# Kernel optimization log

Hardware: AMD Instinct MI355X
Metric: run time of the kernel (lower is better)

Reference implementation:

```python
import jax, jax.numpy as jnp
import numpy as np

WS = 8          # window size
DIM = 512       # channels
NH = 16         # heads
HD = DIM // NH  # head dim = 32
N = WS * WS     # tokens per window = 64
NW = 64         # windows per image
B = 16          # images
BW = B * NW     # total windows = 1024
SCALE = HD ** -0.5


def _relative_position_index():
    # Swin relative position index, shape (N, N), values in [0, (2*WS-1)^2)
    coords = np.stack(np.meshgrid(np.arange(WS), np.arange(WS), indexing='ij'))  # (2, WS, WS)
    coords_flat = coords.reshape(2, -1)                                           # (2, N)
    rel = coords_flat[:, :, None] - coords_flat[:, None, :]                       # (2, N, N)
    rel = rel.transpose(1, 2, 0).astype(np.int32)                                 # (N, N, 2)
    rel[:, :, 0] += WS - 1
    rel[:, :, 1] += WS - 1
    rel[:, :, 0] *= 2 * WS - 1
    return jnp.asarray(rel.sum(-1))                                               # (N, N)


def setup_inputs() -> dict:
    key = jax.random.key(0)
    ks = jax.random.split(key, 7)
    x = jax.random.normal(ks[0], (BW, N, DIM), dtype=jnp.float32)
    mask = jax.random.normal(ks[1], (NW, N, N), dtype=jnp.float32)  # shift mask (additive)
    qkv_w = jax.random.normal(ks[2], (3 * DIM, DIM), dtype=jnp.float32) * 0.02
    qkv_b = jax.random.normal(ks[3], (3 * DIM,), dtype=jnp.float32) * 0.02
    rel_bias_table = jax.random.normal(ks[4], ((2 * WS - 1) ** 2, NH), dtype=jnp.float32) * 0.02
    proj_w = jax.random.normal(ks[5], (DIM, DIM), dtype=jnp.float32) * 0.02
    proj_b = jax.random.normal(ks[6], (DIM,), dtype=jnp.float32) * 0.02
    rel_index = _relative_position_index()
    return {"x": x, "mask": mask, "qkv_w": qkv_w, "qkv_b": qkv_b,
            "rel_bias_table": rel_bias_table, "proj_w": proj_w, "proj_b": proj_b,
            "rel_index": rel_index}


def reference(x, mask, qkv_w, qkv_b, rel_bias_table, proj_w, proj_b, rel_index):
    # qkv projection: (BW, N, 3*DIM) -> (3, BW, NH, N, HD)
    qkv = (x @ qkv_w.T + qkv_b).reshape(BW, N, 3, NH, HD).transpose(2, 0, 3, 1, 4)
    q, k, v = qkv[0], qkv[1], qkv[2]
    # scaled dot-product scores: (BW, NH, N, N)
    attn = jnp.einsum('bhnd,bhmd->bhnm', q * SCALE, k)
    # relative position bias: gather (N*N,) -> (N, N, NH) -> (NH, N, N)
    bias = rel_bias_table[rel_index.reshape(-1)].reshape(N, N, NH).transpose(2, 0, 1)
    attn = attn + bias[None]
    # shift mask: broadcast over images and heads
    attn = attn.reshape(B, NW, NH, N, N) + mask[None, :, None]
    attn = jax.nn.softmax(attn.reshape(BW, NH, N, N), axis=-1)
    # weighted values: (BW, NH, N, HD) -> (BW, N, DIM)
    out = jnp.einsum('bhnm,bhmd->bhnd', attn, v).transpose(0, 2, 1, 3).reshape(BW, N, DIM)
    return out @ proj_w.T + proj_b
```

## Files before the change

kernel.cpp:

```cpp
#include <hip/hip_runtime.h>
#include <hip/hip_bf16.h>

typedef __bf16 bf16;
typedef __bf16 bf16x4 __attribute__((ext_vector_type(4)));
typedef __bf16 bf16x8 __attribute__((ext_vector_type(8)));
typedef float  f32x4  __attribute__((ext_vector_type(4)));

#define AS1 __attribute__((address_space(1)))
#define AS3 __attribute__((address_space(3)))

__device__ __forceinline__ void gld_lds16(const void* g, void* l) {
    __builtin_amdgcn_global_load_lds((AS1 void*)g, (AS3 void*)l, 16, 0, 0);
}

__global__ void cvt_kernel(const float* __restrict__ in, bf16* __restrict__ out,
                           int n4) {
    for (long i = (long)blockIdx.x * blockDim.x + threadIdx.x; i < n4;
         i += (long)gridDim.x * blockDim.x) {
        f32x4 v = ((const f32x4*)in)[i];
        bf16x4 h;
#pragma unroll
        for (int e = 0; e < 4; ++e) h[e] = (bf16)v[e];
        ((bf16x4*)out)[i] = h;
    }
}

__global__ void bias_kernel(const int* __restrict__ rel_index,
                            const float* __restrict__ table,
                            float* __restrict__ bias) {
    int idx = blockIdx.x * 256 + threadIdx.x;
    int rc = idx & 4095;
    int h  = idx >> 12;
    bias[idx] = table[rel_index[rc] * 16 + h];
}

__global__ __launch_bounds__(256) void gemm1_qkv(
    const bf16* __restrict__ A, const bf16* __restrict__ B,
    const float* __restrict__ bias, bf16* __restrict__ Cq,
    bf16* __restrict__ Ckv)
{
    __shared__ __attribute__((aligned(16))) bf16 As[128 * 64];
    __shared__ __attribute__((aligned(16))) bf16 Bs[128 * 64];

    const int t    = threadIdx.x;
    const int w    = t >> 6;
    const int lane = t & 63;
    const int q    = lane >> 4;
    const int r16  = lane & 15;
    const int wm   = (w & 1) * 64;
    const int wn   = (w >> 1) * 64;
    const long bM  = (long)blockIdx.x * 128;
    const long bN  = (long)blockIdx.y * 128;

    const int sRow = lane >> 3;
    const int sCol = (lane & 7) * 8;

    f32x4 acc[4][4];
#pragma unroll
    for (int i = 0; i < 4; ++i)
#pragma unroll
        for (int j = 0; j < 4; ++j)
            acc[i][j] = f32x4{0.f, 0.f, 0.f, 0.f};

    for (int k0 = 0; k0 < 512; k0 += 64) {
#pragma unroll
        for (int it = 0; it < 4; ++it) {
            const int chunk = w * 4 + it;
            const int row   = chunk * 8 + sRow;
            gld_lds16(A + (bM + row) * 512L + k0 + sCol, As + chunk * 512);
            gld_lds16(B + (bN + row) * 512L + k0 + sCol, Bs + chunk * 512);
        }
        asm volatile("s_waitcnt vmcnt(0)" ::: "memory");
        __syncthreads();

#pragma unroll
        for (int ks = 0; ks < 2; ++ks) {
            bf16x8 av[4], bv[4];
#pragma unroll
            for (int i = 0; i < 4; ++i)
                av[i] = *(const bf16x8*)&As[(wm + i * 16 + r16) * 64 + ks * 32 + q * 8];
#pragma unroll
            for (int j = 0; j < 4; ++j)
                bv[j] = *(const bf16x8*)&Bs[(wn + j * 16 + r16) * 64 + ks * 32 + q * 8];
#pragma unroll
            for (int i = 0; i < 4; ++i)
#pragma unroll
                for (int j = 0; j < 4; ++j)
                    acc[i][j] = __builtin_amdgcn_mfma_f32_16x16x32_bf16(
                        av[i], bv[j], acc[i][j], 0, 0, 0);
        }
        __syncthreads();
    }

    const bool isQ = (bN < 512);
#pragma unroll
    for (int j = 0; j < 4; ++j) {
        const long colg = bN + wn + j * 16 + r16;
        const float bvv = bias[colg];
#pragma unroll
        for (int i = 0; i < 4; ++i) {
            const long row = bM + wm + i * 16 + q * 4;
#pragma unroll
            for (int r = 0; r < 4; ++r) {
                const float v = acc[i][j][r] + bvv;
                if (isQ) Cq [(row + r) * 512  + colg]         = (bf16)v;
                else     Ckv[(row + r) * 1024 + (colg - 512)] = (bf16)v;
            }
        }
    }
}

__global__ __launch_bounds__(256) void gemm2_proj(
    const bf16* __restrict__ A, const bf16* __restrict__ B,
    const float* __restrict__ bias, float* __restrict__ C)
{
    __shared__ __attribute__((aligned(16))) bf16 As[128 * 64];
    __shared__ __attribute__((aligned(16))) bf16 Bs[128 * 64];

    const int t    = threadIdx.x;
    const int w    = t >> 6;
    const int lane = t & 63;
    const int q    = lane >> 4;
    const int r16  = lane & 15;
    const int wm   = (w & 1) * 64;
    const int wn   = (w >> 1) * 64;
    const long bM  = (long)blockIdx.x * 128;
    const long bN  = (long)blockIdx.y * 128;

    const int sRow = lane >> 3;
    const int sCol = (lane & 7) * 8;

    f32x4 acc[4][4];
#pragma unroll
    for (int i = 0; i < 4; ++i)
#pragma unroll
        for (int j = 0; j < 4; ++j)
            acc[i][j] = f32x4{0.f, 0.f, 0.f, 0.f};

    for (int k0 = 0; k0 < 512; k0 += 64) {
#pragma unroll
        for (int it = 0; it < 4; ++it) {
            const int chunk = w * 4 + it;
            const int row   = chunk * 8 + sRow;
            gld_lds16(A + (bM + row) * 512L + k0 + sCol, As + chunk * 512);
            gld_lds16(B + (bN + row) * 512L + k0 + sCol, Bs + chunk * 512);
        }
        asm volatile("s_waitcnt vmcnt(0)" ::: "memory");
        __syncthreads();

#pragma unroll
        for (int ks = 0; ks < 2; ++ks) {
            bf16x8 av[4], bv[4];
#pragma unroll
            for (int i = 0; i < 4; ++i)
                av[i] = *(const bf16x8*)&As[(wm + i * 16 + r16) * 64 + ks * 32 + q * 8];
#pragma unroll
            for (int j = 0; j < 4; ++j)
                bv[j] = *(const bf16x8*)&Bs[(wn + j * 16 + r16) * 64 + ks * 32 + q * 8];
#pragma unroll
            for (int i = 0; i < 4; ++i)
#pragma unroll
                for (int j = 0; j < 4; ++j)
                    acc[i][j] = __builtin_amdgcn_mfma_f32_16x16x32_bf16(
                        av[i], bv[j], acc[i][j], 0, 0, 0);
        }
        __syncthreads();
    }

#pragma unroll
    for (int j = 0; j < 4; ++j) {
        const long col = bN + wn + j * 16 + r16;
        const float bvv = bias[col];
#pragma unroll
        for (int i = 0; i < 4; ++i) {
            const long row = bM + wm + i * 16 + q * 4;
#pragma unroll
            for (int r = 0; r < 4; ++r)
                C[(row + r) * 512L + col] = acc[i][j][r] + bvv;
        }
    }
}

__global__ __launch_bounds__(64) void attn_kernel(
    bf16* __restrict__ qbuf, const bf16* __restrict__ kv,
    const float* __restrict__ mask, const float* __restrict__ bias)
{
    __shared__ __attribute__((aligned(16))) bf16 smem[6144];
    bf16* Qs = smem;
    bf16* Ks = smem + 2048;
    bf16* Vt = smem + 4096;
    bf16* Ps = smem;

    const int lane = threadIdx.x;
    const int q    = lane >> 4;
    const int r16  = lane & 15;
    const int bw   = blockIdx.x >> 4;
    const int h    = blockIdx.x & 15;
    const int nw   = bw & 63;
    const long rowbase = (long)bw * 64;

#pragma unroll
    for (int it = 0; it < 4; ++it) {
        const int tok  = it * 16 + (lane >> 2);
        const int part = (lane & 3) * 8;
        gld_lds16(qbuf + (rowbase + tok) * 512  + h * 32 + part, Qs + it * 512);
        gld_lds16(kv   + (rowbase + tok) * 1024 + h * 32 + part, Ks + it * 512);
    }
    {
        const bf16* gv = kv + (rowbase + lane) * 1024 + 512 + h * 32;
        uint4 vtmp[4];
#pragma unroll
        for (int jj = 0; jj < 4; ++jj) vtmp[jj] = ((const uint4*)gv)[jj];
        const bf16* vrow = (const bf16*)vtmp;
#pragma unroll
        for (int hd = 0; hd < 32; ++hd)
            Vt[hd * 64 + lane] = vrow[hd];
    }
    asm volatile("s_waitcnt vmcnt(0)" ::: "memory");
    __syncthreads();

    f32x4 acc[4][4];
    {
        bf16x8 av[4], bv[4];
#pragma unroll
        for (int ti = 0; ti < 4; ++ti)
            av[ti] = *(const bf16x8*)&Qs[(ti * 16 + r16) * 32 + q * 8];
#pragma unroll
        for (int tj = 0; tj < 4; ++tj)
            bv[tj] = *(const bf16x8*)&Ks[(tj * 16 + r16) * 32 + q * 8];
        const f32x4 z = f32x4{0.f, 0.f, 0.f, 0.f};
#pragma unroll
        for (int ti = 0; ti < 4; ++ti)
#pragma unroll
            for (int tj = 0; tj < 4; ++tj)
                acc[ti][tj] = __builtin_amdgcn_mfma_f32_16x16x32_bf16(
                    av[ti], bv[tj], z, 0, 0, 0);
    }

    const float SCALE  = 0.17677669529663687f;
    const float LOG2E  = 1.4426950408889634f;
    const float* biasH = bias + h * 4096;
    const float* maskW = mask + nw * 4096;

#pragma unroll
    for (int ti = 0; ti < 4; ++ti) {
#pragma unroll
        for (int r = 0; r < 4; ++r) {
            const int row = ti * 16 + q * 4 + r;
            float mx = -1e30f;
#pragma unroll
            for (int tj = 0; tj < 4; ++tj) {
                const int col = tj * 16 + r16;
                float s = acc[ti][tj][r] * SCALE
                        + biasH[row * 64 + col] + maskW[row * 64 + col];
                acc[ti][tj][r] = s;
                mx = fmaxf(mx, s);
            }
#pragma unroll
            for (int d = 1; d < 16; d <<= 1)
                mx = fmaxf(mx, __shfl_xor(mx, d, 16));
            float sum = 0.f;
#pragma unroll
            for (int tj = 0; tj < 4; ++tj) {
                float e = exp2f((acc[ti][tj][r] - mx) * LOG2E);
                acc[ti][tj][r] = e;
                sum += e;
            }
#pragma unroll
            for (int d = 1; d < 16; d <<= 1)
                sum += __shfl_xor(sum, d, 16);
            const float inv = 1.0f / sum;
#pragma unroll
            for (int tj = 0; tj < 4; ++tj)
                Ps[row * 64 + tj * 16 + r16] = (bf16)(acc[ti][tj][r] * inv);
        }
    }
    __syncthreads();

    f32x4 o[4][2];
#pragma unroll
    for (int ti = 0; ti < 4; ++ti)
#pragma unroll
        for (int tn = 0; tn < 2; ++tn)
            o[ti][tn] = f32x4{0.f, 0.f, 0.f, 0.f};

#pragma unroll
    for (int ks = 0; ks < 2; ++ks) {
        bf16x8 av[4], bv[2];
#pragma unroll
        for (int ti = 0; ti < 4; ++ti)
            av[ti] = *(const bf16x8*)&Ps[(ti * 16 + r16) * 64 + ks * 32 + q * 8];
#pragma unroll
        for (int tn = 0; tn < 2; ++tn)
            bv[tn] = *(const bf16x8*)&Vt[(tn * 16 + r16) * 64 + ks * 32 + q * 8];
#pragma unroll
        for (int ti = 0; ti < 4; ++ti)
#pragma unroll
            for (int tn = 0; tn < 2; ++tn)
                o[ti][tn] = __builtin_amdgcn_mfma_f32_16x16x32_bf16(
                    av[ti], bv[tn], o[ti][tn], 0, 0, 0);
    }

    bf16* op = qbuf + rowbase * 512 + h * 32;
#pragma unroll
    for (int ti = 0; ti < 4; ++ti)
#pragma unroll
        for (int tn = 0; tn < 2; ++tn)
#pragma unroll
            for (int r = 0; r < 4; ++r)
                op[(long)(ti * 16 + q * 4 + r) * 512 + tn * 16 + r16] =
                    (bf16)(o[ti][tn][r]);
}

extern "C" void kernel_launch(void* const* d_in, const int* in_sizes, int n_in,
                              void* d_out, int out_size, void* d_ws, size_t ws_size,
                              hipStream_t stream) {
    const float* x      = (const float*)d_in[0];
    const float* mask   = (const float*)d_in[1];
    const float* qkv_w  = (const float*)d_in[2];
    const float* qkv_b  = (const float*)d_in[3];
    const float* table  = (const float*)d_in[4];
    const float* proj_w = (const float*)d_in[5];
    const float* proj_b = (const float*)d_in[6];
    const int*   relidx = (const int*)d_in[7];
    float* out = (float*)d_out;

    char*  ws   = (char*)d_ws;
    float* bias = (float*)ws;
    bf16*  qbuf = (bf16*)(ws + 262144);
    bf16*  xbf  = (bf16*)(ws + 67371008);
    bf16*  wq   = (bf16*)(ws + 134479872);
    bf16*  wp   = (bf16*)(ws + 136052736);
    const size_t need_full = 136577024ull + 134217728ull;
    bf16* kvbuf = (ws_size >= need_full) ? (bf16*)(ws + 136577024)
                                         : (bf16*)d_out;

    bias_kernel<<<256, 256, 0, stream>>>(relidx, table, bias);
    cvt_kernel<<<2048, 256, 0, stream>>>(x,      xbf, 8388608);
    cvt_kernel<<<768,  256, 0, stream>>>(qkv_w,  wq,  196608);
    cvt_kernel<<<256,  256, 0, stream>>>(proj_w, wp,  65536);

    gemm1_qkv<<<dim3(512, 12), 256, 0, stream>>>(xbf, wq, qkv_b, qbuf, kvbuf);
    attn_kernel<<<16384, 64, 0, stream>>>(qbuf, kvbuf, mask, bias);
    gemm2_proj<<<dim3(512, 4), 256, 0, stream>>>(qbuf, wp, proj_b, out);
}
```

Before: 617.6 us.

## Rewrite QKV GEMM as 256x256 multi-stage pipelined kernel with LDS-staged epilogue

Replaces the 128x128 single-buffered QKV GEMM with a 256x256 tile, 512-thread kernel. It uses a four-stage global-to-LDS pipeline with interleaved MFMA phases, barriers and priority hints, plus a grouped block-index swizzle for L2 reuse. The epilogue stages results through swizzled LDS so global stores are coalesced 16-byte writes instead of scattered 2-byte ones. It aims to hide load latency and raise MFMA utilisation, at the cost of 128KB of LDS per block and a complex hand-scheduled loop that is fragile to ordering mistakes.

```diff
diff --git a/kernel.cpp b/kernel.cpp
--- a/kernel.cpp
+++ b/kernel.cpp
@@ -34,79 +34,129 @@
     bias[idx] = table[rel_index[rc] * 16 + h];
 }
 
-__global__ __launch_bounds__(256) void gemm1_qkv(
+#define STAGE(GBASE, LBASE, SK0)                                          \
+    { _Pragma("unroll")                                                   \
+      for (int c_ = 0; c_ < 2; ++c_)                                      \
+          gld_lds16((GBASE) + c_ * 16 * 512 + (SK0),                      \
+                    (LBASE) + (w * 2 + c_) * 512); }
+
+#define PHASE(S, KK, IH, LOADB, GB, LB, SK0, VM)                            \
+  {                                                                         \
+    const bf16* ap_ = sA + ((S)*2+(KK))*8192 + (wm128+(IH)*64+r16)*32 + q*8;\
+    _Pragma("unroll")                                                       \
+    for (int ii = 0; ii < 4; ++ii) av[ii] = *(const bf16x8*)(ap_ + ii*512); \
+    if (LOADB) {                                                            \
+      const bf16* bp_ = sB + ((S)*2+(KK))*8192 + (wn64+r16)*32 + q*8;       \
+      _Pragma("unroll")                                                     \
+      for (int jj = 0; jj < 4; ++jj) bv[jj] = *(const bf16x8*)(bp_+jj*512); \
+    }                                                                       \
+    STAGE(GB, LB, SK0);                                                     \
+    __builtin_amdgcn_sched_barrier(0);                                      \
+    __builtin_amdgcn_s_barrier();                                           \
+    asm volatile("s_waitcnt lgkmcnt(0)");                                   \
+    __builtin_amdgcn_sched_barrier(0);                                      \
+    __builtin_amdgcn_s_setprio(1);                                          \
+    _Pragma("unroll")                                                       \
+    for (int ii = 0; ii < 4; ++ii)                                          \
+      _Pragma("unroll")                                                     \
+      for (int jj = 0; jj < 4; ++jj)                                        \
+        acc[(IH)*4+ii][jj] = __builtin_amdgcn_mfma_f32_16x16x32_bf16(       \
+            av[ii], bv[jj], acc[(IH)*4+ii][jj], 0, 0, 0);                   \
+    __builtin_amdgcn_s_setprio(0);                                          \
+    if (VM) asm volatile("s_waitcnt vmcnt(4)");                             \
+    __builtin_amdgcn_sched_barrier(0);                                      \
+    __builtin_amdgcn_s_barrier();                                           \
+  }
+
+__global__ __launch_bounds__(512, 2) void gemm1_qkv8(
     const bf16* __restrict__ A, const bf16* __restrict__ B,
     const float* __restrict__ bias, bf16* __restrict__ Cq,
     bf16* __restrict__ Ckv)
 {
-    __shared__ __attribute__((aligned(16))) bf16 As[128 * 64];
-    __shared__ __attribute__((aligned(16))) bf16 Bs[128 * 64];
-
-    const int t    = threadIdx.x;
-    const int w    = t >> 6;
-    const int lane = t & 63;
-    const int q    = lane >> 4;
-    const int r16  = lane & 15;
-    const int wm   = (w & 1) * 64;
-    const int wn   = (w >> 1) * 64;
-    const long bM  = (long)blockIdx.x * 128;
-    const long bN  = (long)blockIdx.y * 128;
-
-    const int sRow = lane >> 3;
-    const int sCol = (lane & 7) * 8;
-
-    f32x4 acc[4][4];
-#pragma unroll
-    for (int i = 0; i < 4; ++i)
-#pragma unroll
-        for (int j = 0; j < 4; ++j)
-            acc[i][j] = f32x4{0.f, 0.f, 0.f, 0.f};
-
-    for (int k0 = 0; k0 < 512; k0 += 64) {
-#pragma unroll
-        for (int it = 0; it < 4; ++it) {
-            const int chunk = w * 4 + it;
-            const int row   = chunk * 8 + sRow;
-            gld_lds16(A + (bM + row) * 512L + k0 + sCol, As + chunk * 512);
-            gld_lds16(B + (bN + row) * 512L + k0 + sCol, Bs + chunk * 512);
-        }
-        asm volatile("s_waitcnt vmcnt(0)" ::: "memory");
-        __syncthreads();
-
-#pragma unroll
-        for (int ks = 0; ks < 2; ++ks) {
-            bf16x8 av[4], bv[4];
-#pragma unroll
-            for (int i = 0; i < 4; ++i)
-                av[i] = *(const bf16x8*)&As[(wm + i * 16 + r16) * 64 + ks * 32 + q * 8];
-#pragma unroll
-            for (int j = 0; j < 4; ++j)
-                bv[j] = *(const bf16x8*)&Bs[(wn + j * 16 + r16) * 64 + ks * 32 + q * 8];
-#pragma unroll
-            for (int i = 0; i < 4; ++i)
-#pragma unroll
-                for (int j = 0; j < 4; ++j)
-                    acc[i][j] = __builtin_amdgcn_mfma_f32_16x16x32_bf16(
-                        av[i], bv[j], acc[i][j], 0, 0, 0);
-        }
-        __syncthreads();
-    }
+    __shared__ __attribute__((aligned(16))) char smemraw[131072];
+    bf16* sA = (bf16*)smemraw;
+    bf16* sB = sA + 32768;
+
+    const int t     = threadIdx.x;
+    const int w     = t >> 6;
+    const int lane  = t & 63;
+    const int q     = lane >> 4;
+    const int r16   = lane & 15;
+    const int wm128 = (w >> 2) * 128;
+    const int wn64  = (w & 3) * 64;
+
+    const int bid = blockIdx.x;
+    const int wg  = (bid & 7) * 192 + (bid >> 3);
+    const long bM = (long)(wg / 6) * 256;
+    const long bN = (long)(wg % 6) * 256;
+
+    const bf16* Ast = A + (bM + w * 32 + (lane >> 2)) * 512 + (lane & 3) * 8;
+    const bf16* Bst = B + (bN + w * 32 + (lane >> 2)) * 512 + (lane & 3) * 8;
+
+    f32x4 acc[8][4];
+#pragma unroll
+    for (int i = 0; i < 8; ++i)
+#pragma unroll
+        for (int j = 0; j < 4; ++j) acc[i][j] = f32x4{0.f, 0.f, 0.f, 0.f};
+
+    bf16x8 av[4], bv[4];
+
+    STAGE(Ast, sA + 0,     0);
+    STAGE(Bst, sB + 0,     0);
+    STAGE(Ast, sA + 8192,  32);
+    STAGE(Bst, sB + 8192,  32);
+    STAGE(Ast, sA + 16384, 64);
+    STAGE(Bst, sB + 16384, 64);
+    asm volatile("s_waitcnt vmcnt(4)");
+    __builtin_amdgcn_sched_barrier(0);
+    __builtin_amdgcn_s_barrier();
+
+    for (int i = 0; i < 4; ++i) {
+        const int t1 = 2 * i + 1;
+        const int t2 = (2 * i + 2 < 8) ? 2 * i + 2 : 7;
+        const int t3 = (2 * i + 3 < 8) ? 2 * i + 3 : 7;
+        PHASE(0, 0, 0, 1, Ast, sA + 24576, t1 * 64 + 32, 0)
+        PHASE(0, 0, 1, 0, Bst, sB + 24576, t1 * 64 + 32, 0)
+        PHASE(0, 1, 1, 1, Ast, sA + 0,     t2 * 64,      0)
+        PHASE(0, 1, 0, 0, Bst, sB + 0,     t2 * 64,      1)
+        PHASE(1, 0, 0, 1, Ast, sA + 8192,  t2 * 64 + 32, 0)
+        PHASE(1, 0, 1, 0, Bst, sB + 8192,  t2 * 64 + 32, 0)
+        PHASE(1, 1, 1, 1, Ast, sA + 16384, t3 * 64,      0)
+        PHASE(1, 1, 0, 0, Bst, sB + 16384, t3 * 64,      1)
+    }
+
+    asm volatile("s_waitcnt vmcnt(0)");
+    __builtin_amdgcn_sched_barrier(0);
+    __builtin_amdgcn_s_barrier();
+
+    bf16* ct = (bf16*)smemraw;
+#pragma unroll
+    for (int j = 0; j < 4; ++j) {
+        const int col  = wn64 + j * 16 + r16;
+        const float bvv = bias[bN + col];
+        const int chunk = col >> 3, cl = col & 7;
+#pragma unroll
+        for (int i = 0; i < 8; ++i)
+#pragma unroll
+            for (int r = 0; r < 4; ++r) {
+                const int row = wm128 + i * 16 + q * 4 + r;
+                ct[row * 256 + ((chunk ^ ((row >> 2) & 7)) << 3) + cl] =
+                    (bf16)(acc[i][j][r] + bvv);
+            }
+    }
+    __syncthreads();
 
     const bool isQ = (bN < 512);
-#pragma unroll
-    for (int j = 0; j < 4; ++j) {
-        const long colg = bN + wn + j * 16 + r16;
-        const float bvv = bias[colg];
-#pragma unroll
-        for (int i = 0; i < 4; ++i) {
-            const long row = bM + wm + i * 16 + q * 4;
-#pragma unroll
-            for (int r = 0; r < 4; ++r) {
-                const float v = acc[i][j][r] + bvv;
-                if (isQ) Cq [(row + r) * 512  + colg]         = (bf16)v;
-                else     Ckv[(row + r) * 1024 + (colg - 512)] = (bf16)v;
-            }
-        }
+    bf16* __restrict__ outp = isQ ? (Cq + bM * 512 + bN)
+                                  : (Ckv + bM * 1024 + (bN - 512));
+    const int ostr = isQ ? 512 : 1024;
+#pragma unroll
+    for (int it = 0; it < 16; ++it) {
+        const int row = w * 32 + it * 2 + (lane >> 5);
+        const int c   = lane & 31;
+        uint4 v = *(const uint4*)(ct + row * 256 +
+                                  ((c ^ ((row >> 2) & 7)) << 3));
+        *(uint4*)(outp + (long)row * ostr + c * 8) = v;
     }
 }
 
@@ -340,7 +390,7 @@
     cvt_kernel<<<768,  256, 0, stream>>>(qkv_w,  wq,  196608);
     cvt_kernel<<<256,  256, 0, stream>>>(proj_w, wp,  65536);
 
-    gemm1_qkv<<<dim3(512, 12), 256, 0, stream>>>(xbf, wq, qkv_b, qbuf, kvbuf);
+    gemm1_qkv8<<<1536, 512, 0, stream>>>(xbf, wq, qkv_b, qbuf, kvbuf);
     attn_kernel<<<16384, 64, 0, stream>>>(qbuf, kvbuf, mask, bias);
     gemm2_proj<<<dim3(512, 4), 256, 0, stream>>>(qbuf, wp, proj_b, out);
 }
```

Result: faster. 562.0 us (-9.0%).
